# Performance work log

Measured on AMD Instinct MI355X. Metric: run time of the kernel, lower is better.

The kernel has to match this reference:

```python
import jax, jax.numpy as jnp
import numpy as np

DIM = 512
N_HEADS = 8
HEAD_DIM = DIM // N_HEADS


def rope_pos(T, head_dim, dtype=jnp.float32):
    inv_freq = 1.0 / (10000.0 ** (jnp.arange(0, head_dim, 2, dtype=jnp.float32) / head_dim))
    t = jnp.arange(T, dtype=jnp.float32)
    freqs = jnp.einsum('i,j->ij', t, inv_freq)            # [T, head_dim/2]
    return jnp.concatenate([freqs, freqs], axis=-1).astype(dtype)  # [T, head_dim]


def rotate_half(x):
    x1, x2 = jnp.split(x, 2, axis=-1)
    return jnp.concatenate([-x2, x1], axis=-1)


def apply_rope(pos, t):
    # pos: [T, hd] -> broadcast to [1,1,T,hd]; t: [B,H,T,hd]
    pos = pos[None, None, :, :]
    return t * jnp.cos(pos) + rotate_half(t) * jnp.sin(pos)


def setup_inputs() -> dict:
    key = jax.random.key(0)
    ks = jax.random.split(key, 6)
    B, T = 4, 2048
    x = jax.random.normal(ks[0], (B, T, DIM), dtype=jnp.float32)
    mask = jnp.zeros((B, T), dtype=jnp.float32)  # additive mask
    s = 1.0 / np.sqrt(DIM)
    qkv_w = jax.random.normal(ks[1], (3 * DIM, DIM), dtype=jnp.float32) * s
    qkv_b = jnp.zeros((3 * DIM,), dtype=jnp.float32)
    proj_w = jax.random.normal(ks[2], (DIM, DIM), dtype=jnp.float32) * s
    proj_b = jnp.zeros((DIM,), dtype=jnp.float32)
    return {"x": x, "mask": mask, "qkv_w": qkv_w, "qkv_b": qkv_b,
            "proj_w": proj_w, "proj_b": proj_b}


def reference(x, mask, qkv_w, qkv_b, proj_w, proj_b):
    B, T, C = x.shape
    qkv = x @ qkv_w.T + qkv_b                       # [B,T,3C]
    qkv = qkv.reshape(B, T, 3, N_HEADS, HEAD_DIM)
    q, k, v = qkv[:, :, 0], qkv[:, :, 1], qkv[:, :, 2]  # [B,T,H,hd]
    q = q.transpose(0, 2, 1, 3)                     # [B,H,T,hd]
    k = k.transpose(0, 2, 1, 3)
    v = v.transpose(0, 2, 1, 3)
    pos = rope_pos(T, HEAD_DIM, x.dtype)
    q = apply_rope(pos, q)
    k = apply_rope(pos, k)
    scores = jnp.einsum('bhqd,bhkd->bhqk', q, k) * (1.0 / np.sqrt(HEAD_DIM))
    scores = scores + mask[:, None, None, :]        # 2D mask -> [B,1,1,T]
    probs = jax.nn.softmax(scores.astype(jnp.float32), axis=-1).astype(x.dtype)
    # dropout is identity in eval mode
    out = jnp.einsum('bhqk,bhkd->bhqd', probs, v)   # [B,H,T,hd]
    out = out.transpose(0, 2, 1, 3).reshape(B, T, C)
    return out @ proj_w.T + proj_b
```

## Files before the change

kernel.cpp:

```cpp
#include <hip/hip_runtime.h>
#include <math.h>


typedef __attribute__((ext_vector_type(8))) short bf16x8;
typedef __attribute__((ext_vector_type(4))) float floatx4;

#define LOG2E 1.44269504088896f

__device__ __forceinline__ unsigned short f2bf(float f) {
  unsigned int u = __float_as_uint(f);
  u += 0x7fffu + ((u >> 16) & 1u);
  return (unsigned short)(u >> 16);
}

__device__ __forceinline__ void gld_lds16(unsigned short* lds, const unsigned short* g) {
  __builtin_amdgcn_global_load_lds(
      (const __attribute__((address_space(1))) unsigned int*)g,
      (__attribute__((address_space(3))) unsigned int*)lds, 16, 0, 0);
}

__global__ __launch_bounds__(256) void prep_kernel(
    const float* __restrict__ x, const float* __restrict__ wq, const float* __restrict__ wp,
    unsigned short* __restrict__ xb, unsigned short* __restrict__ wqb,
    unsigned short* __restrict__ wpb, float* __restrict__ cosT, float* __restrict__ sinT) {
  int i = blockIdx.x * 256 + threadIdx.x;
  if (i < 4194304) {
    xb[i] = f2bf(x[i]);
  } else if (i < 4980736) {
    int j = i - 4194304; wqb[j] = f2bf(wq[j]);
  } else if (i < 5242880) {
    int j = i - 4980736; wpb[j] = f2bf(wp[j]);
  } else if (i < 5308416) {
    int j = i - 5242880;
    int t = j >> 5, f = j & 31;
    double fr = (double)t * pow(10000.0, -(double)f / 32.0);
    cosT[j] = (float)cos(fr);
    sinT[j] = (float)sin(fr);
  }
}

__global__ __launch_bounds__(256) void qkv_kernel(
    const unsigned short* __restrict__ xb, const unsigned short* __restrict__ wqb,
    const float* __restrict__ qkv_b, const float* __restrict__ cosT,
    const float* __restrict__ sinT, unsigned short* __restrict__ Qb,
    unsigned short* __restrict__ Kb, unsigned short* __restrict__ Vtb) {
  __shared__ __align__(16) unsigned short As[128 * 32];
  __shared__ __align__(16) unsigned short Bs[128 * 32];
  const int tid = threadIdx.x;
  const int wave = tid >> 6, lane = tid & 63, ln = lane & 15, quad = lane >> 4;
  const int m0 = blockIdx.x * 128, n0 = blockIdx.y * 128;
  const int wr = (wave >> 1) * 64, wc = (wave & 1) * 64;

  floatx4 acc[4][4];
#pragma unroll
  for (int i = 0; i < 4; ++i)
#pragma unroll
    for (int j = 0; j < 4; ++j) acc[i][j] = (floatx4){0.f, 0.f, 0.f, 0.f};

  const int c0 = tid, c1 = tid + 256;
  const int ar0 = c0 >> 2, ak0 = (c0 & 3) * 8;
  const int ar1 = c1 >> 2, ak1 = (c1 & 3) * 8;

  for (int k0 = 0; k0 < 512; k0 += 32) {
    __syncthreads();
    gld_lds16(As + c0 * 8, xb + (size_t)(m0 + ar0) * 512 + k0 + ak0);
    gld_lds16(As + c1 * 8, xb + (size_t)(m0 + ar1) * 512 + k0 + ak1);
    gld_lds16(Bs + c0 * 8, wqb + (size_t)(n0 + ar0) * 512 + k0 + ak0);
    gld_lds16(Bs + c1 * 8, wqb + (size_t)(n0 + ar1) * 512 + k0 + ak1);
    __syncthreads();
    bf16x8 af[4], bfb[4];
#pragma unroll
    for (int mi = 0; mi < 4; ++mi)
      af[mi] = *(const bf16x8*)(As + (wr + mi * 16 + ln) * 32 + quad * 8);
#pragma unroll
    for (int ni = 0; ni < 4; ++ni)
      bfb[ni] = *(const bf16x8*)(Bs + (wc + ni * 16 + ln) * 32 + quad * 8);
#pragma unroll
    for (int mi = 0; mi < 4; ++mi)
#pragma unroll
      for (int ni = 0; ni < 4; ++ni)
        acc[mi][ni] = __builtin_amdgcn_mfma_f32_16x16x32_bf16(af[mi], bfb[ni], acc[mi][ni], 0, 0, 0);
  }

  const int colbase = n0 + wc;
  const int mat = colbase >> 9;
  const int h = (colbase & 511) >> 6;
  float bias[4];
#pragma unroll
  for (int ni = 0; ni < 4; ++ni) bias[ni] = qkv_b[colbase + ni * 16 + ln];

  if (mat == 2) {
#pragma unroll
    for (int mi = 0; mi < 4; ++mi) {
      int row0 = m0 + wr + mi * 16 + quad * 4;
      int bidx = row0 >> 11, t = row0 & 2047;
#pragma unroll
      for (int ni = 0; ni < 4; ++ni) {
        int d = ni * 16 + ln;
        ushort4 pk;
        pk.x = f2bf(acc[mi][ni][0] + bias[ni]);
        pk.y = f2bf(acc[mi][ni][1] + bias[ni]);
        pk.z = f2bf(acc[mi][ni][2] + bias[ni]);
        pk.w = f2bf(acc[mi][ni][3] + bias[ni]);
        *(ushort4*)(Vtb + ((size_t)(bidx * 8 + h) * 64 + d) * 2048 + t) = pk;
      }
    }
  } else {
    unsigned short* dst = (mat == 0) ? Qb : Kb;
    const float sc = (mat == 0) ? 0.125f * LOG2E : 1.0f;
#pragma unroll
    for (int mi = 0; mi < 4; ++mi) {
#pragma unroll
      for (int r = 0; r < 4; ++r) {
        int row = m0 + wr + mi * 16 + quad * 4 + r;
        int bidx = row >> 11, t = row & 2047;
        const float* cr = cosT + t * 32;
        const float* sr = sinT + t * 32;
        size_t obase = ((size_t)(bidx * 8 + h) * 2048 + t) * 64;
#pragma unroll
        for (int ni = 0; ni < 2; ++ni) {
          int dlo = ni * 16 + ln;
          float cv = cr[dlo], sv = sr[dlo];
          float xlo = acc[mi][ni][r] + bias[ni];
          float xhi = acc[mi][ni + 2][r] + bias[ni + 2];
          dst[obase + dlo]      = f2bf((xlo * cv - xhi * sv) * sc);
          dst[obase + dlo + 32] = f2bf((xhi * cv + xlo * sv) * sc);
        }
      }
    }
  }
}

__global__ __launch_bounds__(256) void attn_kernel(
    const unsigned short* __restrict__ Qb, const unsigned short* __restrict__ Kb,
    const unsigned short* __restrict__ Vtb, const float* __restrict__ mask,
    unsigned short* __restrict__ attnb) {
  __shared__ __align__(16) unsigned short Ks[64 * 72];
  __shared__ __align__(16) unsigned short Vs[64 * 72];
  __shared__ __align__(16) unsigned short Ps[128 * 72];

  const int tid = threadIdx.x;
  const int wave = tid >> 6, lane = tid & 63, ln = lane & 15, quad = lane >> 4;
  const int bh = blockIdx.y;
  const int b = bh >> 3, h = bh & 7;
  const int wq0 = blockIdx.x * 128 + wave * 32;

  const unsigned short* Qhead = Qb + (size_t)bh * 2048 * 64;
  const unsigned short* Khead = Kb + (size_t)bh * 2048 * 64;
  const unsigned short* Vhead = Vtb + (size_t)bh * 64 * 2048;

  bf16x8 qf[2][2];
#pragma unroll
  for (int ni2 = 0; ni2 < 2; ++ni2)
#pragma unroll
    for (int ks = 0; ks < 2; ++ks)
      qf[ni2][ks] = *(const bf16x8*)(Qhead + (size_t)(wq0 + ni2 * 16 + ln) * 64 + ks * 32 + quad * 8);

  floatx4 o[4][2];
#pragma unroll
  for (int mi2 = 0; mi2 < 4; ++mi2)
#pragma unroll
    for (int ni2 = 0; ni2 < 2; ++ni2) o[mi2][ni2] = (floatx4){0.f, 0.f, 0.f, 0.f};
  float mrun[2] = {-INFINITY, -INFINITY};
  float lrun[2] = {0.f, 0.f};

  const int srow = tid >> 3, soff = (tid & 7) * 8;
  uint4 kpre0 = *(const uint4*)(Khead + (size_t)srow * 64 + soff);
  uint4 kpre1 = *(const uint4*)(Khead + (size_t)(srow + 32) * 64 + soff);
  uint4 vpre0 = *(const uint4*)(Vhead + (size_t)srow * 2048 + soff);
  uint4 vpre1 = *(const uint4*)(Vhead + (size_t)(srow + 32) * 2048 + soff);

  for (int k0 = 0; k0 < 2048; k0 += 64) {
    __syncthreads();
    *(uint4*)(Ks + srow * 72 + soff) = kpre0;
    *(uint4*)(Ks + (srow + 32) * 72 + soff) = kpre1;
    *(uint4*)(Vs + srow * 72 + soff) = vpre0;
    *(uint4*)(Vs + (srow + 32) * 72 + soff) = vpre1;
    __syncthreads();
    if (k0 + 64 < 2048) {
      kpre0 = *(const uint4*)(Khead + (size_t)(k0 + 64 + srow) * 64 + soff);
      kpre1 = *(const uint4*)(Khead + (size_t)(k0 + 64 + srow + 32) * 64 + soff);
      vpre0 = *(const uint4*)(Vhead + (size_t)srow * 2048 + k0 + 64 + soff);
      vpre1 = *(const uint4*)(Vhead + (size_t)(srow + 32) * 2048 + k0 + 64 + soff);
    }

    floatx4 sm[4][2];
#pragma unroll
    for (int mi = 0; mi < 4; ++mi) {
      bf16x8 kf0 = *(const bf16x8*)(Ks + (mi * 16 + ln) * 72 + quad * 8);
      bf16x8 kf1 = *(const bf16x8*)(Ks + (mi * 16 + ln) * 72 + 32 + quad * 8);
#pragma unroll
      for (int ni2 = 0; ni2 < 2; ++ni2) {
        floatx4 a = (floatx4){0.f, 0.f, 0.f, 0.f};
        a = __builtin_amdgcn_mfma_f32_16x16x32_bf16(kf0, qf[ni2][0], a, 0, 0, 0);
        a = __builtin_amdgcn_mfma_f32_16x16x32_bf16(kf1, qf[ni2][1], a, 0, 0, 0);
        sm[mi][ni2] = a;
      }
    }
#pragma unroll
    for (int mi = 0; mi < 4; ++mi) {
      float4 mv = *(const float4*)(mask + b * 2048 + k0 + mi * 16 + quad * 4);
      float m0v = mv.x * LOG2E, m1v = mv.y * LOG2E, m2v = mv.z * LOG2E, m3v = mv.w * LOG2E;
#pragma unroll
      for (int ni2 = 0; ni2 < 2; ++ni2) {
        sm[mi][ni2][0] += m0v; sm[mi][ni2][1] += m1v;
        sm[mi][ni2][2] += m2v; sm[mi][ni2][3] += m3v;
      }
    }
    float alpha[2];
#pragma unroll
    for (int ni2 = 0; ni2 < 2; ++ni2) {
      float vmax = sm[0][ni2][0];
#pragma unroll
      for (int mi = 0; mi < 4; ++mi)
#pragma unroll
        for (int r = 0; r < 4; ++r) vmax = fmaxf(vmax, sm[mi][ni2][r]);
      vmax = fmaxf(vmax, __shfl_xor(vmax, 16));
      vmax = fmaxf(vmax, __shfl_xor(vmax, 32));
      float nm = fmaxf(mrun[ni2], vmax);
      alpha[ni2] = exp2f(mrun[ni2] - nm);
      mrun[ni2] = nm;
    }
    float psum[2] = {0.f, 0.f};
#pragma unroll
    for (int mi = 0; mi < 4; ++mi)
#pragma unroll
      for (int ni2 = 0; ni2 < 2; ++ni2)
#pragma unroll
        for (int r = 0; r < 4; ++r) {
          float p = exp2f(sm[mi][ni2][r] - mrun[ni2]);
          sm[mi][ni2][r] = p;
          psum[ni2] += p;
        }
#pragma unroll
    for (int ni2 = 0; ni2 < 2; ++ni2) {
      float s = psum[ni2];
      s += __shfl_xor(s, 16);
      s += __shfl_xor(s, 32);
      lrun[ni2] = lrun[ni2] * alpha[ni2] + s;
    }
#pragma unroll
    for (int mi2 = 0; mi2 < 4; ++mi2)
#pragma unroll
      for (int ni2 = 0; ni2 < 2; ++ni2) {
        o[mi2][ni2][0] *= alpha[ni2]; o[mi2][ni2][1] *= alpha[ni2];
        o[mi2][ni2][2] *= alpha[ni2]; o[mi2][ni2][3] *= alpha[ni2];
      }
#pragma unroll
    for (int mi = 0; mi < 4; ++mi)
#pragma unroll
      for (int ni2 = 0; ni2 < 2; ++ni2) {
        ushort4 pk;
        pk.x = f2bf(sm[mi][ni2][0]); pk.y = f2bf(sm[mi][ni2][1]);
        pk.z = f2bf(sm[mi][ni2][2]); pk.w = f2bf(sm[mi][ni2][3]);
        *(ushort4*)(Ps + (wq0 - blockIdx.x * 128 + ni2 * 16 + ln) * 72 + mi * 16 + quad * 4) = pk;
      }
#pragma unroll
    for (int ks = 0; ks < 2; ++ks) {
      bf16x8 pb[2];
#pragma unroll
      for (int ni2 = 0; ni2 < 2; ++ni2)
        pb[ni2] = *(const bf16x8*)(Ps + (wave * 32 + ni2 * 16 + ln) * 72 + ks * 32 + quad * 8);
#pragma unroll
      for (int mi2 = 0; mi2 < 4; ++mi2) {
        bf16x8 vf = *(const bf16x8*)(Vs + (mi2 * 16 + ln) * 72 + ks * 32 + quad * 8);
#pragma unroll
        for (int ni2 = 0; ni2 < 2; ++ni2)
          o[mi2][ni2] = __builtin_amdgcn_mfma_f32_16x16x32_bf16(vf, pb[ni2], o[mi2][ni2], 0, 0, 0);
      }
    }
  }

#pragma unroll
  for (int ni2 = 0; ni2 < 2; ++ni2) {
    float inv = 1.f / lrun[ni2];
    int t = wq0 + ni2 * 16 + ln;
    size_t base = ((size_t)b * 2048 + t) * 512 + h * 64;
#pragma unroll
    for (int mi2 = 0; mi2 < 4; ++mi2) {
      ushort4 pk;
      pk.x = f2bf(o[mi2][ni2][0] * inv); pk.y = f2bf(o[mi2][ni2][1] * inv);
      pk.z = f2bf(o[mi2][ni2][2] * inv); pk.w = f2bf(o[mi2][ni2][3] * inv);
      *(ushort4*)(attnb + base + mi2 * 16 + quad * 4) = pk;
    }
  }
}

__global__ __launch_bounds__(256) void proj_kernel(
    const unsigned short* __restrict__ ab, const unsigned short* __restrict__ wpb,
    const float* __restrict__ proj_b, float* __restrict__ out) {
  __shared__ __align__(16) unsigned short As[128 * 32];
  __shared__ __align__(16) unsigned short Bs[128 * 32];
  const int tid = threadIdx.x;
  const int wave = tid >> 6, lane = tid & 63, ln = lane & 15, quad = lane >> 4;
  const int m0 = blockIdx.x * 128, n0 = blockIdx.y * 128;
  const int wr = (wave >> 1) * 64, wc = (wave & 1) * 64;

  floatx4 acc[4][4];
#pragma unroll
  for (int i = 0; i < 4; ++i)
#pragma unroll
    for (int j = 0; j < 4; ++j) acc[i][j] = (floatx4){0.f, 0.f, 0.f, 0.f};

  const int c0 = tid, c1 = tid + 256;
  const int ar0 = c0 >> 2, ak0 = (c0 & 3) * 8;
  const int ar1 = c1 >> 2, ak1 = (c1 & 3) * 8;

  for (int k0 = 0; k0 < 512; k0 += 32) {
    __syncthreads();
    gld_lds16(As + c0 * 8, ab + (size_t)(m0 + ar0) * 512 + k0 + ak0);
    gld_lds16(As + c1 * 8, ab + (size_t)(m0 + ar1) * 512 + k0 + ak1);
    gld_lds16(Bs + c0 * 8, wpb + (size_t)(n0 + ar0) * 512 + k0 + ak0);
    gld_lds16(Bs + c1 * 8, wpb + (size_t)(n0 + ar1) * 512 + k0 + ak1);
    __syncthreads();
    bf16x8 af[4], bfb[4];
#pragma unroll
    for (int mi = 0; mi < 4; ++mi)
      af[mi] = *(const bf16x8*)(As + (wr + mi * 16 + ln) * 32 + quad * 8);
#pragma unroll
    for (int ni = 0; ni < 4; ++ni)
      bfb[ni] = *(const bf16x8*)(Bs + (wc + ni * 16 + ln) * 32 + quad * 8);
#pragma unroll
    for (int mi = 0; mi < 4; ++mi)
#pragma unroll
      for (int ni = 0; ni < 4; ++ni)
        acc[mi][ni] = __builtin_amdgcn_mfma_f32_16x16x32_bf16(af[mi], bfb[ni], acc[mi][ni], 0, 0, 0);
  }

#pragma unroll
  for (int mi = 0; mi < 4; ++mi)
#pragma unroll
    for (int ni = 0; ni < 4; ++ni) {
      int col = n0 + wc + ni * 16 + ln;
      float pb = proj_b[col];
#pragma unroll
      for (int r = 0; r < 4; ++r) {
        int row = m0 + wr + mi * 16 + quad * 4 + r;
        out[(size_t)row * 512 + col] = acc[mi][ni][r] + pb;
      }
    }
}

extern "C" void kernel_launch(void* const* d_in, const int* in_sizes, int n_in,
                              void* d_out, int out_size, void* d_ws, size_t ws_size,
                              hipStream_t stream) {
  const float* x      = (const float*)d_in[0];
  const float* mask   = (const float*)d_in[1];
  const float* qkv_w  = (const float*)d_in[2];
  const float* qkv_b  = (const float*)d_in[3];
  const float* proj_w = (const float*)d_in[4];
  const float* proj_b = (const float*)d_in[5];
  float* out = (float*)d_out;

  char* ws = (char*)d_ws;
  unsigned short* xb   = (unsigned short*)(ws);
  unsigned short* wqb  = (unsigned short*)(ws + 8388608);
  unsigned short* wpb  = (unsigned short*)(ws + 9961472);
  float* cosT          = (float*)(ws + 10485760);
  float* sinT          = (float*)(ws + 10747904);
  unsigned short* Qb   = (unsigned short*)(ws + 11010048);
  unsigned short* Kb   = (unsigned short*)(ws + 19398656);
  unsigned short* Vtb  = (unsigned short*)(ws + 27787264);
  unsigned short* attnb= (unsigned short*)(ws + 36175872);

  prep_kernel<<<20736, 256, 0, stream>>>(x, qkv_w, proj_w, xb, wqb, wpb, cosT, sinT);
  dim3 g1(64, 12);
  qkv_kernel<<<g1, 256, 0, stream>>>(xb, wqb, qkv_b, cosT, sinT, Qb, Kb, Vtb);
  dim3 g2(16, 32);
  attn_kernel<<<g2, 256, 0, stream>>>(Qb, Kb, Vtb, mask, attnb);
  dim3 g3(64, 4);
  proj_kernel<<<g3, 256, 0, stream>>>(attnb, wpb, proj_b, out);
}
```

Baseline: 212.0 us.

## Split attention KV range across waves, read K/V directly, vectorize epilogues

The attention kernel now gives each 128-thread block 32 queries and splits the 2048 keys between two waves, which are then merged with a log-sum-exp combine through shared memory. K and V fragments are loaded straight from global memory instead of being staged in LDS behind block barriers. The mask is folded into the MFMA accumulator init, and row sums are computed with a ones-vector MFMA. Separately, the QKV and projection GEMMs swap their MFMA operands so the epilogues can write packed, vectorized bf16 and float4 stores, using a packed bf16 conversion builtin when it exists. These changes aim to raise attention parallelism, remove barriers and scalar stores, but they rely on cache reuse for the global K/V reads and add a cross-wave merge step.

```diff
diff --git a/kernel.cpp b/kernel.cpp
--- a/kernel.cpp
+++ b/kernel.cpp
@@ -11,6 +11,23 @@
   unsigned int u = __float_as_uint(f);
   u += 0x7fffu + ((u >> 16) & 1u);
   return (unsigned short)(u >> 16);
+}
+
+#if defined(__has_builtin)
+#if __has_builtin(__builtin_amdgcn_cvt_pk_bf16_f32)
+#define HAVE_PK_BF16 1
+#endif
+#endif
+
+__device__ __forceinline__ unsigned int f2bf2(float a, float b) {
+#ifdef HAVE_PK_BF16
+  auto v = __builtin_amdgcn_cvt_pk_bf16_f32(a, b);
+  union { decltype(v) x; unsigned int u; } c;
+  c.x = v;
+  return c.u;
+#else
+  return (unsigned int)f2bf(a) | ((unsigned int)f2bf(b) << 16);
+#endif
 }
 
 __device__ __forceinline__ void gld_lds16(unsigned short* lds, const unsigned short* g) {
@@ -50,6 +67,7 @@
   const int wave = tid >> 6, lane = tid & 63, ln = lane & 15, quad = lane >> 4;
   const int m0 = blockIdx.x * 128, n0 = blockIdx.y * 128;
   const int wr = (wave >> 1) * 64, wc = (wave & 1) * 64;
+  const bool isV = (blockIdx.y >= 8);
 
   floatx4 acc[4][4];
 #pragma unroll
@@ -75,21 +93,29 @@
 #pragma unroll
     for (int ni = 0; ni < 4; ++ni)
       bfb[ni] = *(const bf16x8*)(Bs + (wc + ni * 16 + ln) * 32 + quad * 8);
-#pragma unroll
-    for (int mi = 0; mi < 4; ++mi)
-#pragma unroll
-      for (int ni = 0; ni < 4; ++ni)
-        acc[mi][ni] = __builtin_amdgcn_mfma_f32_16x16x32_bf16(af[mi], bfb[ni], acc[mi][ni], 0, 0, 0);
+    if (isV) {
+#pragma unroll
+      for (int mi = 0; mi < 4; ++mi)
+#pragma unroll
+        for (int ni = 0; ni < 4; ++ni)
+          acc[mi][ni] = __builtin_amdgcn_mfma_f32_16x16x32_bf16(af[mi], bfb[ni], acc[mi][ni], 0, 0, 0);
+    } else {
+#pragma unroll
+      for (int mi = 0; mi < 4; ++mi)
+#pragma unroll
+        for (int ni = 0; ni < 4; ++ni)
+          acc[mi][ni] = __builtin_amdgcn_mfma_f32_16x16x32_bf16(bfb[mi], af[ni], acc[mi][ni], 0, 0, 0);
+    }
   }
 
   const int colbase = n0 + wc;
   const int mat = colbase >> 9;
   const int h = (colbase & 511) >> 6;
-  float bias[4];
-#pragma unroll
-  for (int ni = 0; ni < 4; ++ni) bias[ni] = qkv_b[colbase + ni * 16 + ln];
-
-  if (mat == 2) {
+
+  if (isV) {
+    float bias[4];
+#pragma unroll
+    for (int ni = 0; ni < 4; ++ni) bias[ni] = qkv_b[colbase + ni * 16 + ln];
 #pragma unroll
     for (int mi = 0; mi < 4; ++mi) {
       int row0 = m0 + wr + mi * 16 + quad * 4;
@@ -97,148 +123,119 @@
 #pragma unroll
       for (int ni = 0; ni < 4; ++ni) {
         int d = ni * 16 + ln;
-        ushort4 pk;
-        pk.x = f2bf(acc[mi][ni][0] + bias[ni]);
-        pk.y = f2bf(acc[mi][ni][1] + bias[ni]);
-        pk.z = f2bf(acc[mi][ni][2] + bias[ni]);
-        pk.w = f2bf(acc[mi][ni][3] + bias[ni]);
-        *(ushort4*)(Vtb + ((size_t)(bidx * 8 + h) * 64 + d) * 2048 + t) = pk;
+        unsigned int u0 = f2bf2(acc[mi][ni][0] + bias[ni], acc[mi][ni][1] + bias[ni]);
+        unsigned int u1 = f2bf2(acc[mi][ni][2] + bias[ni], acc[mi][ni][3] + bias[ni]);
+        *(uint2*)(Vtb + ((size_t)(bidx * 8 + h) * 64 + d) * 2048 + t) = make_uint2(u0, u1);
       }
     }
   } else {
     unsigned short* dst = (mat == 0) ? Qb : Kb;
     const float sc = (mat == 0) ? 0.125f * LOG2E : 1.0f;
-#pragma unroll
-    for (int mi = 0; mi < 4; ++mi) {
-#pragma unroll
-      for (int r = 0; r < 4; ++r) {
-        int row = m0 + wr + mi * 16 + quad * 4 + r;
-        int bidx = row >> 11, t = row & 2047;
-        const float* cr = cosT + t * 32;
-        const float* sr = sinT + t * 32;
-        size_t obase = ((size_t)(bidx * 8 + h) * 2048 + t) * 64;
-#pragma unroll
-        for (int ni = 0; ni < 2; ++ni) {
-          int dlo = ni * 16 + ln;
-          float cv = cr[dlo], sv = sr[dlo];
-          float xlo = acc[mi][ni][r] + bias[ni];
-          float xhi = acc[mi][ni + 2][r] + bias[ni + 2];
-          dst[obase + dlo]      = f2bf((xlo * cv - xhi * sv) * sc);
-          dst[obase + dlo + 32] = f2bf((xhi * cv + xlo * sv) * sc);
-        }
-      }
-    }
-  }
-}
-
-__global__ __launch_bounds__(256) void attn_kernel(
+    float4 blo[2], bhi[2];
+#pragma unroll
+    for (int mi = 0; mi < 2; ++mi) {
+      blo[mi] = *(const float4*)(qkv_b + colbase + mi * 16 + quad * 4);
+      bhi[mi] = *(const float4*)(qkv_b + colbase + 32 + mi * 16 + quad * 4);
+    }
+#pragma unroll
+    for (int ni = 0; ni < 4; ++ni) {
+      int row = m0 + wr + ni * 16 + ln;
+      int bidx = row >> 11, t = row & 2047;
+      unsigned short* tb = dst + ((size_t)(bidx * 8 + h) * 2048 + t) * 64;
+#pragma unroll
+      for (int mi = 0; mi < 2; ++mi) {
+        int dbase = mi * 16 + quad * 4;
+        float4 c4 = *(const float4*)(cosT + t * 32 + dbase);
+        float4 s4 = *(const float4*)(sinT + t * 32 + dbase);
+        float xl0 = acc[mi][ni][0] + blo[mi].x, xh0 = acc[mi + 2][ni][0] + bhi[mi].x;
+        float xl1 = acc[mi][ni][1] + blo[mi].y, xh1 = acc[mi + 2][ni][1] + bhi[mi].y;
+        float xl2 = acc[mi][ni][2] + blo[mi].z, xh2 = acc[mi + 2][ni][2] + bhi[mi].z;
+        float xl3 = acc[mi][ni][3] + blo[mi].w, xh3 = acc[mi + 2][ni][3] + bhi[mi].w;
+        unsigned int lo01 = f2bf2((xl0 * c4.x - xh0 * s4.x) * sc, (xl1 * c4.y - xh1 * s4.y) * sc);
+        unsigned int lo23 = f2bf2((xl2 * c4.z - xh2 * s4.z) * sc, (xl3 * c4.w - xh3 * s4.w) * sc);
+        unsigned int hi01 = f2bf2((xh0 * c4.x + xl0 * s4.x) * sc, (xh1 * c4.y + xl1 * s4.y) * sc);
+        unsigned int hi23 = f2bf2((xh2 * c4.z + xl2 * s4.z) * sc, (xh3 * c4.w + xl3 * s4.w) * sc);
+        *(uint2*)(tb + dbase) = make_uint2(lo01, lo23);
+        *(uint2*)(tb + 32 + dbase) = make_uint2(hi01, hi23);
+      }
+    }
+  }
+}
+
+__global__ __launch_bounds__(128, 4) void attn_kernel(
     const unsigned short* __restrict__ Qb, const unsigned short* __restrict__ Kb,
     const unsigned short* __restrict__ Vtb, const float* __restrict__ mask,
     unsigned short* __restrict__ attnb) {
-  __shared__ __align__(16) unsigned short Ks[64 * 72];
-  __shared__ __align__(16) unsigned short Vs[64 * 72];
-  __shared__ __align__(16) unsigned short Ps[128 * 72];
+  __shared__ __align__(16) unsigned short Ps[2 * 32 * 72];
+  __shared__ __align__(16) float Om[8 * 64 * 4];
+  __shared__ float Ml[4 * 64];
 
   const int tid = threadIdx.x;
   const int wave = tid >> 6, lane = tid & 63, ln = lane & 15, quad = lane >> 4;
   const int bh = blockIdx.y;
   const int b = bh >> 3, h = bh & 7;
-  const int wq0 = blockIdx.x * 128 + wave * 32;
+  const int q0 = blockIdx.x * 32;
+  const int kbeg = wave * 1024;
 
   const unsigned short* Qhead = Qb + (size_t)bh * 2048 * 64;
   const unsigned short* Khead = Kb + (size_t)bh * 2048 * 64;
   const unsigned short* Vhead = Vtb + (size_t)bh * 64 * 2048;
+  unsigned short* Pw = Ps + wave * 32 * 72;
 
   bf16x8 qf[2][2];
 #pragma unroll
   for (int ni2 = 0; ni2 < 2; ++ni2)
 #pragma unroll
     for (int ks = 0; ks < 2; ++ks)
-      qf[ni2][ks] = *(const bf16x8*)(Qhead + (size_t)(wq0 + ni2 * 16 + ln) * 64 + ks * 32 + quad * 8);
+      qf[ni2][ks] = *(const bf16x8*)(Qhead + (size_t)(q0 + ni2 * 16 + ln) * 64 + ks * 32 + quad * 8);
+
+  bf16x8 ones;
+#pragma unroll
+  for (int j = 0; j < 8; ++j) ones[j] = (short)0x3F80;
 
   floatx4 o[4][2];
 #pragma unroll
   for (int mi2 = 0; mi2 < 4; ++mi2)
 #pragma unroll
     for (int ni2 = 0; ni2 < 2; ++ni2) o[mi2][ni2] = (floatx4){0.f, 0.f, 0.f, 0.f};
+  floatx4 o5[2] = {(floatx4){0.f, 0.f, 0.f, 0.f}, (floatx4){0.f, 0.f, 0.f, 0.f}};
   float mrun[2] = {-INFINITY, -INFINITY};
-  float lrun[2] = {0.f, 0.f};
-
-  const int srow = tid >> 3, soff = (tid & 7) * 8;
-  uint4 kpre0 = *(const uint4*)(Khead + (size_t)srow * 64 + soff);
-  uint4 kpre1 = *(const uint4*)(Khead + (size_t)(srow + 32) * 64 + soff);
-  uint4 vpre0 = *(const uint4*)(Vhead + (size_t)srow * 2048 + soff);
-  uint4 vpre1 = *(const uint4*)(Vhead + (size_t)(srow + 32) * 2048 + soff);
-
-  for (int k0 = 0; k0 < 2048; k0 += 64) {
-    __syncthreads();
-    *(uint4*)(Ks + srow * 72 + soff) = kpre0;
-    *(uint4*)(Ks + (srow + 32) * 72 + soff) = kpre1;
-    *(uint4*)(Vs + srow * 72 + soff) = vpre0;
-    *(uint4*)(Vs + (srow + 32) * 72 + soff) = vpre1;
-    __syncthreads();
-    if (k0 + 64 < 2048) {
-      kpre0 = *(const uint4*)(Khead + (size_t)(k0 + 64 + srow) * 64 + soff);
-      kpre1 = *(const uint4*)(Khead + (size_t)(k0 + 64 + srow + 32) * 64 + soff);
-      vpre0 = *(const uint4*)(Vhead + (size_t)srow * 2048 + k0 + 64 + soff);
-      vpre1 = *(const uint4*)(Vhead + (size_t)(srow + 32) * 2048 + k0 + 64 + soff);
-    }
-
+
+  for (int k0 = kbeg; k0 < kbeg + 1024; k0 += 64) {
+    floatx4 cini[4];
+#pragma unroll
+    for (int mi = 0; mi < 4; ++mi) {
+      float4 mv = *(const float4*)(mask + b * 2048 + k0 + mi * 16 + quad * 4);
+      cini[mi] = (floatx4){mv.x * LOG2E, mv.y * LOG2E, mv.z * LOG2E, mv.w * LOG2E};
+    }
     floatx4 sm[4][2];
 #pragma unroll
     for (int mi = 0; mi < 4; ++mi) {
-      bf16x8 kf0 = *(const bf16x8*)(Ks + (mi * 16 + ln) * 72 + quad * 8);
-      bf16x8 kf1 = *(const bf16x8*)(Ks + (mi * 16 + ln) * 72 + 32 + quad * 8);
+      bf16x8 kf0 = *(const bf16x8*)(Khead + (size_t)(k0 + mi * 16 + ln) * 64 + quad * 8);
+      bf16x8 kf1 = *(const bf16x8*)(Khead + (size_t)(k0 + mi * 16 + ln) * 64 + 32 + quad * 8);
 #pragma unroll
       for (int ni2 = 0; ni2 < 2; ++ni2) {
-        floatx4 a = (floatx4){0.f, 0.f, 0.f, 0.f};
+        floatx4 a = cini[mi];
         a = __builtin_amdgcn_mfma_f32_16x16x32_bf16(kf0, qf[ni2][0], a, 0, 0, 0);
         a = __builtin_amdgcn_mfma_f32_16x16x32_bf16(kf1, qf[ni2][1], a, 0, 0, 0);
         sm[mi][ni2] = a;
       }
     }
-#pragma unroll
-    for (int mi = 0; mi < 4; ++mi) {
-      float4 mv = *(const float4*)(mask + b * 2048 + k0 + mi * 16 + quad * 4);
-      float m0v = mv.x * LOG2E, m1v = mv.y * LOG2E, m2v = mv.z * LOG2E, m3v = mv.w * LOG2E;
-#pragma unroll
-      for (int ni2 = 0; ni2 < 2; ++ni2) {
-        sm[mi][ni2][0] += m0v; sm[mi][ni2][1] += m1v;
-        sm[mi][ni2][2] += m2v; sm[mi][ni2][3] += m3v;
-      }
-    }
     float alpha[2];
 #pragma unroll
     for (int ni2 = 0; ni2 < 2; ++ni2) {
-      float vmax = sm[0][ni2][0];
-#pragma unroll
-      for (int mi = 0; mi < 4; ++mi)
-#pragma unroll
-        for (int r = 0; r < 4; ++r) vmax = fmaxf(vmax, sm[mi][ni2][r]);
+      float vmax = fmaxf(fmaxf(sm[0][ni2][0], sm[0][ni2][1]), fmaxf(sm[0][ni2][2], sm[0][ni2][3]));
+#pragma unroll
+      for (int mi = 1; mi < 4; ++mi) {
+        vmax = fmaxf(vmax, fmaxf(fmaxf(sm[mi][ni2][0], sm[mi][ni2][1]),
+                                 fmaxf(sm[mi][ni2][2], sm[mi][ni2][3])));
+      }
       vmax = fmaxf(vmax, __shfl_xor(vmax, 16));
       vmax = fmaxf(vmax, __shfl_xor(vmax, 32));
       float nm = fmaxf(mrun[ni2], vmax);
       alpha[ni2] = exp2f(mrun[ni2] - nm);
       mrun[ni2] = nm;
     }
-    float psum[2] = {0.f, 0.f};
-#pragma unroll
-    for (int mi = 0; mi < 4; ++mi)
-#pragma unroll
-      for (int ni2 = 0; ni2 < 2; ++ni2)
-#pragma unroll
-        for (int r = 0; r < 4; ++r) {
-          float p = exp2f(sm[mi][ni2][r] - mrun[ni2]);
-          sm[mi][ni2][r] = p;
-          psum[ni2] += p;
-        }
-#pragma unroll
-    for (int ni2 = 0; ni2 < 2; ++ni2) {
-      float s = psum[ni2];
-      s += __shfl_xor(s, 16);
-      s += __shfl_xor(s, 32);
-      lrun[ni2] = lrun[ni2] * alpha[ni2] + s;
-    }
 #pragma unroll
     for (int mi2 = 0; mi2 < 4; ++mi2)
 #pragma unroll
@@ -247,41 +244,71 @@
         o[mi2][ni2][2] *= alpha[ni2]; o[mi2][ni2][3] *= alpha[ni2];
       }
 #pragma unroll
+    for (int ni2 = 0; ni2 < 2; ++ni2) {
+      o5[ni2][0] *= alpha[ni2]; o5[ni2][1] *= alpha[ni2];
+      o5[ni2][2] *= alpha[ni2]; o5[ni2][3] *= alpha[ni2];
+    }
+#pragma unroll
     for (int mi = 0; mi < 4; ++mi)
 #pragma unroll
       for (int ni2 = 0; ni2 < 2; ++ni2) {
-        ushort4 pk;
-        pk.x = f2bf(sm[mi][ni2][0]); pk.y = f2bf(sm[mi][ni2][1]);
-        pk.z = f2bf(sm[mi][ni2][2]); pk.w = f2bf(sm[mi][ni2][3]);
-        *(ushort4*)(Ps + (wq0 - blockIdx.x * 128 + ni2 * 16 + ln) * 72 + mi * 16 + quad * 4) = pk;
+        unsigned int u0 = f2bf2(exp2f(sm[mi][ni2][0] - mrun[ni2]), exp2f(sm[mi][ni2][1] - mrun[ni2]));
+        unsigned int u1 = f2bf2(exp2f(sm[mi][ni2][2] - mrun[ni2]), exp2f(sm[mi][ni2][3] - mrun[ni2]));
+        *(uint2*)(Pw + (ni2 * 16 + ln) * 72 + mi * 16 + quad * 4) = make_uint2(u0, u1);
       }
 #pragma unroll
     for (int ks = 0; ks < 2; ++ks) {
       bf16x8 pb[2];
 #pragma unroll
       for (int ni2 = 0; ni2 < 2; ++ni2)
-        pb[ni2] = *(const bf16x8*)(Ps + (wave * 32 + ni2 * 16 + ln) * 72 + ks * 32 + quad * 8);
+        pb[ni2] = *(const bf16x8*)(Pw + (ni2 * 16 + ln) * 72 + ks * 32 + quad * 8);
 #pragma unroll
       for (int mi2 = 0; mi2 < 4; ++mi2) {
-        bf16x8 vf = *(const bf16x8*)(Vs + (mi2 * 16 + ln) * 72 + ks * 32 + quad * 8);
+        bf16x8 vf = *(const bf16x8*)(Vhead + (size_t)(mi2 * 16 + ln) * 2048 + k0 + ks * 32 + quad * 8);
 #pragma unroll
         for (int ni2 = 0; ni2 < 2; ++ni2)
           o[mi2][ni2] = __builtin_amdgcn_mfma_f32_16x16x32_bf16(vf, pb[ni2], o[mi2][ni2], 0, 0, 0);
       }
-    }
-  }
-
-#pragma unroll
-  for (int ni2 = 0; ni2 < 2; ++ni2) {
-    float inv = 1.f / lrun[ni2];
-    int t = wq0 + ni2 * 16 + ln;
-    size_t base = ((size_t)b * 2048 + t) * 512 + h * 64;
-#pragma unroll
-    for (int mi2 = 0; mi2 < 4; ++mi2) {
-      ushort4 pk;
-      pk.x = f2bf(o[mi2][ni2][0] * inv); pk.y = f2bf(o[mi2][ni2][1] * inv);
-      pk.z = f2bf(o[mi2][ni2][2] * inv); pk.w = f2bf(o[mi2][ni2][3] * inv);
-      *(ushort4*)(attnb + base + mi2 * 16 + quad * 4) = pk;
+#pragma unroll
+      for (int ni2 = 0; ni2 < 2; ++ni2)
+        o5[ni2] = __builtin_amdgcn_mfma_f32_16x16x32_bf16(ones, pb[ni2], o5[ni2], 0, 0, 0);
+    }
+  }
+
+  if (wave == 0) {
+#pragma unroll
+    for (int mi2 = 0; mi2 < 4; ++mi2)
+#pragma unroll
+      for (int ni2 = 0; ni2 < 2; ++ni2)
+        *(floatx4*)(Om + ((mi2 * 2 + ni2) * 64 + lane) * 4) = o[mi2][ni2];
+#pragma unroll
+    for (int ni2 = 0; ni2 < 2; ++ni2) {
+      Ml[ni2 * 64 + lane] = mrun[ni2];
+      Ml[128 + ni2 * 64 + lane] = o5[ni2][0];
+    }
+  }
+  __syncthreads();
+  if (wave == 1) {
+#pragma unroll
+    for (int ni2 = 0; ni2 < 2; ++ni2) {
+      float m0s = Ml[ni2 * 64 + lane];
+      float l0s = Ml[128 + ni2 * 64 + lane];
+      float M = fmaxf(m0s, mrun[ni2]);
+      float c0 = exp2f(m0s - M);
+      float c1 = exp2f(mrun[ni2] - M);
+      float inv = 1.f / (l0s * c0 + o5[ni2][0] * c1);
+      float ic0 = c0 * inv, ic1 = c1 * inv;
+      int t = q0 + ni2 * 16 + ln;
+      size_t base = ((size_t)b * 2048 + t) * 512 + h * 64;
+#pragma unroll
+      for (int mi2 = 0; mi2 < 4; ++mi2) {
+        floatx4 p0 = *(const floatx4*)(Om + ((mi2 * 2 + ni2) * 64 + lane) * 4);
+        unsigned int u0 = f2bf2(p0[0] * ic0 + o[mi2][ni2][0] * ic1,
+                                p0[1] * ic0 + o[mi2][ni2][1] * ic1);
+        unsigned int u1 = f2bf2(p0[2] * ic0 + o[mi2][ni2][2] * ic1,
+                                p0[3] * ic0 + o[mi2][ni2][3] * ic1);
+        *(uint2*)(attnb + base + mi2 * 16 + quad * 4) = make_uint2(u0, u1);
+      }
     }
   }
 }
@@ -324,21 +351,27 @@
     for (int mi = 0; mi < 4; ++mi)
 #pragma unroll
       for (int ni = 0; ni < 4; ++ni)
-        acc[mi][ni] = __builtin_amdgcn_mfma_f32_16x16x32_bf16(af[mi], bfb[ni], acc[mi][ni], 0, 0, 0);
-  }
-
+        acc[mi][ni] = __builtin_amdgcn_mfma_f32_16x16x32_bf16(bfb[mi], af[ni], acc[mi][ni], 0, 0, 0);
+  }
+
+  float4 bias4[4];
 #pragma unroll
   for (int mi = 0; mi < 4; ++mi)
-#pragma unroll
-    for (int ni = 0; ni < 4; ++ni) {
-      int col = n0 + wc + ni * 16 + ln;
-      float pb = proj_b[col];
-#pragma unroll
-      for (int r = 0; r < 4; ++r) {
-        int row = m0 + wr + mi * 16 + quad * 4 + r;
-        out[(size_t)row * 512 + col] = acc[mi][ni][r] + pb;
-      }
-    }
+    bias4[mi] = *(const float4*)(proj_b + n0 + wc + mi * 16 + quad * 4);
+#pragma unroll
+  for (int ni = 0; ni < 4; ++ni) {
+    int t = m0 + wr + ni * 16 + ln;
+#pragma unroll
+    for (int mi = 0; mi < 4; ++mi) {
+      int col = n0 + wc + mi * 16 + quad * 4;
+      float4 st;
+      st.x = acc[mi][ni][0] + bias4[mi].x;
+      st.y = acc[mi][ni][1] + bias4[mi].y;
+      st.z = acc[mi][ni][2] + bias4[mi].z;
+      st.w = acc[mi][ni][3] + bias4[mi].w;
+      *(float4*)(out + (size_t)t * 512 + col) = st;
+    }
+  }
 }
 
 extern "C" void kernel_launch(void* const* d_in, const int* in_sizes, int n_in,
@@ -366,8 +399,8 @@
   prep_kernel<<<20736, 256, 0, stream>>>(x, qkv_w, proj_w, xb, wqb, wpb, cosT, sinT);
   dim3 g1(64, 12);
   qkv_kernel<<<g1, 256, 0, stream>>>(xb, wqb, qkv_b, cosT, sinT, Qb, Kb, Vtb);
-  dim3 g2(16, 32);
-  attn_kernel<<<g2, 256, 0, stream>>>(Qb, Kb, Vtb, mask, attnb);
+  dim3 g2(64, 32);
+  attn_kernel<<<g2, 128, 0, stream>>>(Qb, Kb, Vtb, mask, attnb);
   dim3 g3(64, 4);
   proj_kernel<<<g3, 256, 0, stream>>>(attnb, wpb, proj_b, out);
 }
```

New measurement: 267.0 us. 25.9% more time.
